# Optimization experiments

Hardware: AMD Instinct MI355X
Metric: run time of the kernel (lower is better)

Reference implementation:

```python
import jax, jax.numpy as jnp
import numpy as np

INNER = 4
AFFECT_W = 0.3
LN_EPS = 1e-5


def _ln(x, w, b):
    m = x.mean(-1, keepdims=True)
    v = ((x - m) ** 2).mean(-1, keepdims=True)
    return (x - m) * jax.lax.rsqrt(v + LN_EPS) * w + b


def _gelu(x):
    return jax.nn.gelu(x, approximate=False)  # torch default erf GELU


def setup_inputs() -> dict:
    key = jax.random.key(0)
    ks = jax.random.split(key, 24)
    B, D = 32768, 128
    s = 0.02
    inp = {
        "x": jax.random.normal(ks[0], (B, D), jnp.float32),
        "y_init": jax.random.normal(ks[1], (B, D), jnp.float32),
        "affect_vec": jax.random.normal(ks[2], (B, 3), jnp.float32),
        # LayerNorms
        "ln_lat_w": jnp.ones((3 * D,), jnp.float32), "ln_lat_b": jnp.zeros((3 * D,), jnp.float32),
        "ln_ans_w": jnp.ones((2 * D,), jnp.float32), "ln_ans_b": jnp.zeros((2 * D,), jnp.float32),
        "ln_z_w": jnp.ones((D,), jnp.float32), "ln_z_b": jnp.zeros((D,), jnp.float32),
        # latent MLP: 3D -> 2D -> D
        "W_lat1": jax.random.normal(ks[3], (3 * D, 2 * D), jnp.float32) * s, "b_lat1": jnp.zeros((2 * D,), jnp.float32),
        "W_lat2": jax.random.normal(ks[4], (2 * D, D), jnp.float32) * s, "b_lat2": jnp.zeros((D,), jnp.float32),
        # answer MLP: 2D -> 2D -> D
        "W_ans1": jax.random.normal(ks[5], (2 * D, 2 * D), jnp.float32) * s, "b_ans1": jnp.zeros((2 * D,), jnp.float32),
        "W_ans2": jax.random.normal(ks[6], (2 * D, D), jnp.float32) * s, "b_ans2": jnp.zeros((D,), jnp.float32),
        # affect proj 3 -> D (tanh), gate 2D -> 1 (sigmoid)
        "W_ap": jax.random.normal(ks[7], (3, D), jnp.float32) * s, "b_ap": jnp.zeros((D,), jnp.float32),
        "W_ag": jax.random.normal(ks[8], (2 * D, 1), jnp.float32) * s, "b_ag": jnp.zeros((1,), jnp.float32),
        # tiny single-head self-attention (q,k,v projections)
        "Wq": jax.random.normal(ks[9], (D, D), jnp.float32) * s, "bq": jnp.zeros((D,), jnp.float32),
        "Wk": jax.random.normal(ks[10], (D, D), jnp.float32) * s, "bk": jnp.zeros((D,), jnp.float32),
        "Wv": jax.random.normal(ks[11], (D, D), jnp.float32) * s, "bv": jnp.zeros((D,), jnp.float32),
        "W_p1": jax.random.normal(ks[12], (D, D // 2), jnp.float32) * s, "b_p1": jnp.zeros((D // 2,), jnp.float32),
        "W_p2": jax.random.normal(ks[13], (D // 2, 3), jnp.float32) * s, "b_p2": jnp.zeros((3,), jnp.float32),
        "K": 5,
    }
    return inp


def reference(x, y_init, affect_vec,
              ln_lat_w, ln_lat_b, ln_ans_w, ln_ans_b, ln_z_w, ln_z_b,
              W_lat1, b_lat1, W_lat2, b_lat2,
              W_ans1, b_ans1, W_ans2, b_ans2,
              W_ap, b_ap, W_ag, b_ag,
              Wq, bq, Wk, bk, Wv, bv,
              W_p1, b_p1, W_p2, b_p2, K):
    D = x.shape[-1]
    scale = 1.0 / jnp.sqrt(jnp.asarray(D, x.dtype))
    y = y_init
    z = jnp.zeros_like(y)
    confs = []
    history = []  # list of [B,1,D]
    for k in range(K):
        for n in range(INNER):
            li = _ln(jnp.concatenate([x, y, z], axis=-1), ln_lat_w, ln_lat_b)
            z_delta = _gelu(li @ W_lat1 + b_lat1) @ W_lat2 + b_lat2
            z = _ln(z + 0.3 * z_delta, ln_z_w, ln_z_b)
        affect_latent = jnp.tanh(affect_vec @ W_ap + b_ap)          # [B,D]
        gate = jax.nn.sigmoid(jnp.concatenate([z, affect_latent], axis=-1) @ W_ag + b_ag)  # [B,1]
        z = z + AFFECT_W * gate * affect_latent
        confs.append(gate.mean())
        history.append(z[:, None, :])
        if len(history) > 1:
            seq = jnp.concatenate(history, axis=1)                   # [B,t,D], t<=K
            q = seq @ Wq + bq
            kk = seq @ Wk + bk
            v = seq @ Wv + bv
            att = jax.nn.softmax(jnp.einsum('btd,bsd->bts', q, kk) * scale, axis=-1)
            attn_out = jnp.einsum('bts,bsd->btd', att, v)
            z = _ln(z + attn_out[:, -1, :], ln_z_w, ln_z_b)
        ai = _ln(jnp.concatenate([y, z], axis=-1), ln_ans_w, ln_ans_b)
        y = y + 0.4 * (_gelu(ai @ W_ans1 + b_ans1) @ W_ans2 + b_ans2)
    pad = jnp.tanh(_gelu(z @ W_p1 + b_p1) @ W_p2 + b_p2)             # [B,3]
    return y, jnp.stack(confs), pad
```

## Files before the change

kernel.cpp:

```cpp
#include <hip/hip_runtime.h>
#include <hip/hip_bf16.h>
#include <math.h>


constexpr int NB = 32768;
constexpr int ND = 128;
constexpr float LNEPS = 1e-5f;

typedef short bf16x8 __attribute__((ext_vector_type(8)));
typedef float f32x4 __attribute__((ext_vector_type(4)));
typedef unsigned uint4v __attribute__((ext_vector_type(4)));
using bf16 = __hip_bfloat16;

static __device__ __forceinline__ float gelu_erf(float x) {
  return 0.5f * x * (1.0f + erff(x * 0.70710678118654752440f));
}
static __device__ __forceinline__ float sigmoidf_(float x) {
  return 1.0f / (1.0f + expf(-x));
}
static __device__ __forceinline__ f32x4 mfma16(bf16x8 a, bf16x8 b, f32x4 c) {
  return __builtin_amdgcn_mfma_f32_16x16x32_bf16(a, b, c, 0, 0, 0);
}
static __device__ __forceinline__ float bfs2f(short u) {
  unsigned v = ((unsigned)(unsigned short)u) << 16;
  return __builtin_bit_cast(float, v);
}
static __device__ __forceinline__ unsigned pk_bf2(float a, float b) {
  unsigned ua = __builtin_bit_cast(unsigned, a);
  unsigned ub = __builtin_bit_cast(unsigned, b);
  ua = (ua + 0x7fffu + ((ua >> 16) & 1u)) >> 16;
  ub = (ub + 0x7fffu + ((ub >> 16) & 1u)) & 0xffff0000u;
  return ub | ua;
}

__global__ void prep_w_frag(const float* __restrict__ src, bf16* __restrict__ dst,
                            int K, int N) {
  int i = blockIdx.x * 256 + threadIdx.x;
  if (i >= K * N) return;
  int k = i / N, n = i - k * N;
  int f = ((n >> 4) * (K >> 5) + (k >> 5)) * 512 + (n & 15) * 32 + (k & 31);
  dst[f] = __float2bfloat16(src[i]);
}

__global__ void prep_w1p(const float* __restrict__ W1, const float* __restrict__ lnw,
                         bf16* __restrict__ WXY, bf16* __restrict__ WZ) {
  int i = blockIdx.x * 256 + threadIdx.x;
  if (i >= 384 * 256) return;
  int j = i >> 8, n = i & 255;
  float v = lnw[j] * W1[i];
  if (j < 256) {
    int f = ((n >> 4) * 8 + (j >> 5)) * 512 + (n & 15) * 32 + (j & 31);
    WXY[f] = __float2bfloat16(v);
  } else {
    int k = j - 256;
    int f = ((n >> 4) * 4 + (k >> 5)) * 512 + (n & 15) * 32 + (k & 31);
    WZ[f] = __float2bfloat16(v);
  }
}

__global__ void prep_uv(const float* __restrict__ W1, const float* __restrict__ lnw,
                        const float* __restrict__ lnb, const float* __restrict__ b1,
                        float* __restrict__ U, float* __restrict__ V0b) {
  int n = threadIdx.x;
  float u = 0.f, v = 0.f;
  for (int j = 0; j < 384; ++j) {
    float w = W1[j * 256 + n];
    u = fmaf(lnw[j], w, u);
    v = fmaf(lnb[j], w, v);
  }
  U[n] = u;
  V0b[n] = v + b1[n];
}

__global__ __launch_bounds__(512) void trm_step(
    const float* __restrict__ x, float* __restrict__ y,
    float* __restrict__ z,
    const bf16* __restrict__ W1XYF, const bf16* __restrict__ W1ZF,
    const float* __restrict__ U, const float* __restrict__ V0b,
    const bf16* __restrict__ W2F, const float* __restrict__ b2,
    const float* __restrict__ lzw, const float* __restrict__ lzb,
    const float* __restrict__ av_g,
    const float* __restrict__ lnw_ans, const float* __restrict__ lnb_ans,
    const bf16* __restrict__ WA1F, const float* __restrict__ ba1,
    const bf16* __restrict__ WA2F, const float* __restrict__ ba2,
    const float* __restrict__ Wap, const float* __restrict__ bap,
    const float* __restrict__ Wag, const float* __restrict__ bag,
    const bf16* __restrict__ WqF, const float* __restrict__ bq,
    const bf16* __restrict__ WkF, const float* __restrict__ bk,
    const bf16* __restrict__ WvF, const float* __restrict__ bv,
    float* __restrict__ gate_sum,
    bf16* __restrict__ kh, bf16* __restrict__ vh, int k)
{
  __shared__ __align__(16) char pool[153600];
  __shared__ float gsum[8];
  float (* const zs)[132] = (float(*)[132])pool;
  float (* const ys)[132] = (float(*)[132])(pool + 33792);
  char* const scr = pool + 67584;
  bf16* const pxy  = (bf16*)scr;
  bf16* const znbL = (bf16*)(scr + 33792);
  bf16* const hx   = (bf16*)(scr + 51200);
  bf16* const znbT = (bf16*)scr;
  bf16* const qvb  = (bf16*)(scr + 17408);
  bf16* const kcb  = (bf16*)(scr + 34816);
  bf16* const vcb  = (bf16*)(scr + 52224);
  bf16* const ai   = (bf16*)scr;
  bf16* const ha   = (bf16*)(scr + 33792);
  float2* const sxy = (float2*)(pool + 152576);
  float2* const mr  = (float2*)(pool + 153088);

  const int t = threadIdx.x;
  const int wave = t >> 6, lane = t & 63;
  const int row8 = t >> 3, sub8 = t & 7;
  const int arow = lane & 15, kseg = (lane >> 4) * 8, crow = (lane >> 4) * 4;
  const size_t row0 = (size_t)blockIdx.x * 64;
  const size_t gr = row0 + row8;

  {
    float s = 0.f, ss = 0.f;
    float4 xv[4], yv[4];
    const float4* xp = (const float4*)&x[gr * ND + sub8 * 16];
    const float4* yp = (const float4*)&y[gr * ND + sub8 * 16];
#pragma unroll
    for (int q = 0; q < 4; ++q) { xv[q] = xp[q]; yv[q] = yp[q]; }
#pragma unroll
    for (int q = 0; q < 4; ++q) {
      s += xv[q].x + xv[q].y + xv[q].z + xv[q].w +
           yv[q].x + yv[q].y + yv[q].z + yv[q].w;
      ss += xv[q].x * xv[q].x + xv[q].y * xv[q].y + xv[q].z * xv[q].z + xv[q].w * xv[q].w +
            yv[q].x * yv[q].x + yv[q].y * yv[q].y + yv[q].z * yv[q].z + yv[q].w * yv[q].w;
    }
#pragma unroll
    for (int q = 0; q < 4; ++q) {
      *(unsigned*)&hx[row8 * 264 + sub8 * 16 + q * 4]       = pk_bf2(xv[q].x, xv[q].y);
      *(unsigned*)&hx[row8 * 264 + sub8 * 16 + q * 4 + 2]   = pk_bf2(xv[q].z, xv[q].w);
      *(unsigned*)&hx[row8 * 264 + 128 + sub8 * 16 + q * 4]     = pk_bf2(yv[q].x, yv[q].y);
      *(unsigned*)&hx[row8 * 264 + 128 + sub8 * 16 + q * 4 + 2] = pk_bf2(yv[q].z, yv[q].w);
      *(float4*)&ys[row8][sub8 * 16 + q * 4] = yv[q];
    }
#pragma unroll
    for (int o = 1; o < 8; o <<= 1) { s += __shfl_xor(s, o); ss += __shfl_xor(ss, o); }

    float zsum = 0.f, zss = 0.f;
    float4 zv[4];
    const float4* zp = (const float4*)&z[gr * ND + sub8 * 16];
#pragma unroll
    for (int q = 0; q < 4; ++q) zv[q] = zp[q];
#pragma unroll
    for (int q = 0; q < 4; ++q) {
      *(float4*)&zs[row8][sub8 * 16 + q * 4] = zv[q];
      *(unsigned*)&znbL[row8 * 136 + sub8 * 16 + q * 4]     = pk_bf2(zv[q].x, zv[q].y);
      *(unsigned*)&znbL[row8 * 136 + sub8 * 16 + q * 4 + 2] = pk_bf2(zv[q].z, zv[q].w);
      zsum += zv[q].x + zv[q].y + zv[q].z + zv[q].w;
      zss += zv[q].x * zv[q].x + zv[q].y * zv[q].y + zv[q].z * zv[q].z + zv[q].w * zv[q].w;
    }
#pragma unroll
    for (int o = 1; o < 8; o <<= 1) { zsum += __shfl_xor(zsum, o); zss += __shfl_xor(zss, o); }
    if (sub8 == 0) {
      sxy[row8] = make_float2(s, ss);
      float mm = (s + zsum) * (1.f / 384.f);
      float var = (ss + zss) * (1.f / 384.f) - mm * mm;
      mr[row8] = make_float2(mm, rsqrtf(var + LNEPS));
    }
  }
  __syncthreads();

  {
    f32x4 acc[4][2];
#pragma unroll
    for (int mi = 0; mi < 4; ++mi)
#pragma unroll
      for (int ni = 0; ni < 2; ++ni) acc[mi][ni] = (f32x4){0.f, 0.f, 0.f, 0.f};
#pragma unroll
    for (int kt = 0; kt < 8; ++kt) {
      bf16x8 a[4];
#pragma unroll
      for (int mi = 0; mi < 4; ++mi)
        a[mi] = *(const bf16x8*)&hx[(mi * 16 + arow) * 264 + kt * 32 + kseg];
#pragma unroll
      for (int ni = 0; ni < 2; ++ni) {
        bf16x8 b = *(const bf16x8*)&W1XYF[(size_t)((wave * 2 + ni) * 8 + kt) * 512 +
                                          arow * 32 + kseg];
        acc[0][ni] = mfma16(a[0], b, acc[0][ni]);
        acc[1][ni] = mfma16(a[1], b, acc[1][ni]);
        acc[2][ni] = mfma16(a[2], b, acc[2][ni]);
        acc[3][ni] = mfma16(a[3], b, acc[3][ni]);
      }
    }
#pragma unroll
    for (int ni = 0; ni < 2; ++ni) {
      int col = (wave * 2 + ni) * 16 + arow;
#pragma unroll
      for (int mi = 0; mi < 4; ++mi)
#pragma unroll
        for (int r = 0; r < 4; ++r)
          pxy[(mi * 16 + crow + r) * 264 + col] = __float2bfloat16(acc[mi][ni][r]);
    }
  }
  __syncthreads();

  float Uv[2], Vv[2];
#pragma unroll
  for (int ni = 0; ni < 2; ++ni) {
    int col = (wave * 2 + ni) * 16 + arow;
    Uv[ni] = U[col];
    Vv[ni] = V0b[col];
  }
  const float b2v = b2[wave * 16 + arow];

  for (int n = 0; n < 4; ++n) {
    {
      f32x4 acc[4][2];
#pragma unroll
      for (int mi = 0; mi < 4; ++mi)
#pragma unroll
        for (int ni = 0; ni < 2; ++ni) acc[mi][ni] = (f32x4){0.f, 0.f, 0.f, 0.f};
#pragma unroll
      for (int kt = 0; kt < 4; ++kt) {
        bf16x8 a[4];
#pragma unroll
        for (int mi = 0; mi < 4; ++mi)
          a[mi] = *(const bf16x8*)&znbL[(mi * 16 + arow) * 136 + kt * 32 + kseg];
#pragma unroll
        for (int ni = 0; ni < 2; ++ni) {
          bf16x8 b = *(const bf16x8*)&W1ZF[(size_t)((wave * 2 + ni) * 4 + kt) * 512 +
                                           arow * 32 + kseg];
          acc[0][ni] = mfma16(a[0], b, acc[0][ni]);
          acc[1][ni] = mfma16(a[1], b, acc[1][ni]);
          acc[2][ni] = mfma16(a[2], b, acc[2][ni]);
          acc[3][ni] = mfma16(a[3], b, acc[3][ni]);
        }
      }
#pragma unroll
      for (int ni = 0; ni < 2; ++ni) {
        int col = (wave * 2 + ni) * 16 + arow;
#pragma unroll
        for (int mi = 0; mi < 4; ++mi)
#pragma unroll
          for (int r = 0; r < 4; ++r) {
            int row = mi * 16 + crow + r;
            float2 mrv = mr[row];
            float pv = __bfloat162float(pxy[row * 264 + col]);
            float hpre = mrv.y * (acc[mi][ni][r] + pv - mrv.x * Uv[ni]) + Vv[ni];
            hx[row * 264 + col] = __float2bfloat16(gelu_erf(hpre));
          }
      }
    }
    __syncthreads();

    {
      f32x4 acc2[4];
#pragma unroll
      for (int mi = 0; mi < 4; ++mi) acc2[mi] = (f32x4){0.f, 0.f, 0.f, 0.f};
#pragma unroll
      for (int kt = 0; kt < 8; ++kt) {
        bf16x8 b = *(const bf16x8*)&W2F[(size_t)(wave * 8 + kt) * 512 + arow * 32 + kseg];
#pragma unroll
        for (int mi = 0; mi < 4; ++mi) {
          bf16x8 a = *(const bf16x8*)&hx[(mi * 16 + arow) * 264 + kt * 32 + kseg];
          acc2[mi] = mfma16(a, b, acc2[mi]);
        }
      }
      int col = wave * 16 + arow;
#pragma unroll
      for (int mi = 0; mi < 4; ++mi)
#pragma unroll
        for (int r = 0; r < 4; ++r)
          zs[mi * 16 + crow + r][col] += 0.3f * (acc2[mi][r] + b2v);
    }
    __syncthreads();

    {
      float4 v[4];
#pragma unroll
      for (int q = 0; q < 4; ++q) v[q] = *(const float4*)&zs[row8][sub8 * 16 + q * 4];
      float s = 0.f, ss = 0.f;
#pragma unroll
      for (int q = 0; q < 4; ++q) {
        s += v[q].x + v[q].y + v[q].z + v[q].w;
        ss += v[q].x * v[q].x + v[q].y * v[q].y + v[q].z * v[q].z + v[q].w * v[q].w;
      }
#pragma unroll
      for (int o = 1; o < 8; o <<= 1) { s += __shfl_xor(s, o); ss += __shfl_xor(ss, o); }
      float m = s * (1.f / 128.f);
      float rstd = rsqrtf(ss * (1.f / 128.f) - m * m + LNEPS);
      float os = 0.f, oss = 0.f;
#pragma unroll
      for (int q = 0; q < 4; ++q) {
        float4 w = *(const float4*)&lzw[sub8 * 16 + q * 4];
        float4 b = *(const float4*)&lzb[sub8 * 16 + q * 4];
        float4 o4;
        o4.x = (v[q].x - m) * rstd * w.x + b.x;
        o4.y = (v[q].y - m) * rstd * w.y + b.y;
        o4.z = (v[q].z - m) * rstd * w.z + b.z;
        o4.w = (v[q].w - m) * rstd * w.w + b.w;
        *(float4*)&zs[row8][sub8 * 16 + q * 4] = o4;
        *(unsigned*)&znbL[row8 * 136 + sub8 * 16 + q * 4]     = pk_bf2(o4.x, o4.y);
        *(unsigned*)&znbL[row8 * 136 + sub8 * 16 + q * 4 + 2] = pk_bf2(o4.z, o4.w);
        os += o4.x + o4.y + o4.z + o4.w;
        oss += o4.x * o4.x + o4.y * o4.y + o4.z * o4.z + o4.w * o4.w;
      }
#pragma unroll
      for (int o = 1; o < 8; o <<= 1) { os += __shfl_xor(os, o); oss += __shfl_xor(oss, o); }
      if (sub8 == 0) {
        float2 sv = sxy[row8];
        float mm = (sv.x + os) * (1.f / 384.f);
        float var = (sv.y + oss) * (1.f / 384.f) - mm * mm;
        mr[row8] = make_float2(mm, rsqrtf(var + LNEPS));
      }
    }
    __syncthreads();
  }

  {
    float zf[16];
#pragma unroll
    for (int q = 0; q < 4; ++q) {
      float4 v = *(const float4*)&zs[row8][sub8 * 16 + q * 4];
      zf[q * 4 + 0] = v.x; zf[q * 4 + 1] = v.y;
      zf[q * 4 + 2] = v.z; zf[q * 4 + 3] = v.w;
    }
    float a0 = av_g[gr * 3 + 0], a1 = av_g[gr * 3 + 1], a2 = av_g[gr * 3 + 2];
    float alf[16];
    float s = 0.f;
#pragma unroll
    for (int e = 0; e < 16; ++e) {
      int c = sub8 * 16 + e;
      alf[e] = tanhf(fmaf(a0, Wap[c], fmaf(a1, Wap[128 + c], fmaf(a2, Wap[256 + c], bap[c]))));
      s += zf[e] * Wag[c] + alf[e] * Wag[128 + c];
    }
#pragma unroll
    for (int o = 1; o < 8; o <<= 1) s += __shfl_xor(s, o);
    float g = sigmoidf_(s + bag[0]);
    float gv = (sub8 == 0) ? g : 0.f;
#pragma unroll
    for (int o = 1; o < 64; o <<= 1) gv += __shfl_xor(gv, o);
    if (lane == 0) gsum[wave] = gv;
#pragma unroll
    for (int e = 0; e < 16; ++e) zf[e] = fmaf(0.3f * g, alf[e], zf[e]);
#pragma unroll
    for (int q = 0; q < 4; ++q) {
      float4 o4;
      o4.x = zf[q * 4 + 0]; o4.y = zf[q * 4 + 1];
      o4.z = zf[q * 4 + 2]; o4.w = zf[q * 4 + 3];
      *(float4*)&zs[row8][sub8 * 16 + q * 4] = o4;
      *(unsigned*)&znbT[row8 * 136 + sub8 * 16 + q * 4]     = pk_bf2(o4.x, o4.y);
      *(unsigned*)&znbT[row8 * 136 + sub8 * 16 + q * 4 + 2] = pk_bf2(o4.z, o4.w);
    }
  }
  __syncthreads();
  if (t == 0) {
    float gs = 0.f;
#pragma unroll
    for (int w = 0; w < 8; ++w) gs += gsum[w];
    atomicAdd(gate_sum + k, gs);
  }

  {
    f32x4 aq[4], ak[4], av2[4];
#pragma unroll
    for (int mi = 0; mi < 4; ++mi) {
      aq[mi] = (f32x4){0.f, 0.f, 0.f, 0.f};
      ak[mi] = (f32x4){0.f, 0.f, 0.f, 0.f};
      av2[mi] = (f32x4){0.f, 0.f, 0.f, 0.f};
    }
#pragma unroll
    for (int kt = 0; kt < 4; ++kt) {
      size_t wr = (size_t)(wave * 4 + kt) * 512 + arow * 32 + kseg;
      bf16x8 bqv = *(const bf16x8*)&WqF[wr];
      bf16x8 bkv = *(const bf16x8*)&WkF[wr];
      bf16x8 bvv = *(const bf16x8*)&WvF[wr];
#pragma unroll
      for (int mi = 0; mi < 4; ++mi) {
        bf16x8 a = *(const bf16x8*)&znbT[(mi * 16 + arow) * 136 + kt * 32 + kseg];
        aq[mi] = mfma16(a, bqv, aq[mi]);
        ak[mi] = mfma16(a, bkv, ak[mi]);
        av2[mi] = mfma16(a, bvv, av2[mi]);
      }
    }
    int col = wave * 16 + arow;
    float bqs = bq[col], bks = bk[col], bvs = bv[col];
#pragma unroll
    for (int mi = 0; mi < 4; ++mi)
#pragma unroll
      for (int r = 0; r < 4; ++r) {
        int row = mi * 16 + crow + r;
        qvb[row * 136 + col] = __float2bfloat16(aq[mi][r] + bqs);
        kcb[row * 136 + col] = __float2bfloat16(ak[mi][r] + bks);
        vcb[row * 136 + col] = __float2bfloat16(av2[mi][r] + bvs);
      }
  }
  __syncthreads();

  if (k < 4) {
    uint4v k0 = *(const uint4v*)&kcb[row8 * 136 + sub8 * 16];
    uint4v k1 = *(const uint4v*)&kcb[row8 * 136 + sub8 * 16 + 8];
    uint4v v0 = *(const uint4v*)&vcb[row8 * 136 + sub8 * 16];
    uint4v v1 = *(const uint4v*)&vcb[row8 * 136 + sub8 * 16 + 8];
    size_t off = ((size_t)k * NB + gr) * ND + sub8 * 16;
    __builtin_nontemporal_store(k0, (uint4v*)&kh[off]);
    __builtin_nontemporal_store(k1, (uint4v*)&kh[off + 8]);
    __builtin_nontemporal_store(v0, (uint4v*)&vh[off]);
    __builtin_nontemporal_store(v1, (uint4v*)&vh[off + 8]);
  }
  {
    float zf[16];
#pragma unroll
    for (int q = 0; q < 4; ++q) {
      float4 v = *(const float4*)&zs[row8][sub8 * 16 + q * 4];
      zf[q * 4 + 0] = v.x; zf[q * 4 + 1] = v.y;
      zf[q * 4 + 2] = v.z; zf[q * 4 + 3] = v.w;
    }
    if (k > 0) {
      bf16x8 qv0 = *(const bf16x8*)&qvb[row8 * 136 + sub8 * 16];
      bf16x8 qv1 = *(const bf16x8*)&qvb[row8 * 136 + sub8 * 16 + 8];
      float p[5];
#pragma unroll
      for (int s = 0; s < 5; ++s) {
        if (s > k) break;
        bf16x8 k0, k1;
        if (s == k) {
          k0 = *(const bf16x8*)&kcb[row8 * 136 + sub8 * 16];
          k1 = *(const bf16x8*)&kcb[row8 * 136 + sub8 * 16 + 8];
        } else {
          size_t off = ((size_t)s * NB + gr) * ND + sub8 * 16;
          k0 = __builtin_bit_cast(bf16x8, __builtin_nontemporal_load((const uint4v*)&kh[off]));
          k1 = __builtin_bit_cast(bf16x8, __builtin_nontemporal_load((const uint4v*)&kh[off + 8]));
        }
        float d = 0.f;
#pragma unroll
        for (int e = 0; e < 8; ++e)
          d += bfs2f(qv0[e]) * bfs2f(k0[e]) + bfs2f(qv1[e]) * bfs2f(k1[e]);
#pragma unroll
        for (int o = 1; o < 8; o <<= 1) d += __shfl_xor(d, o);
        p[s] = d * 0.088388347648318447f;
      }
      float mx = p[0];
#pragma unroll
      for (int s = 1; s < 5; ++s) if (s <= k) mx = fmaxf(mx, p[s]);
      float sum = 0.f;
#pragma unroll
      for (int s = 0; s < 5; ++s) if (s <= k) { p[s] = expf(p[s] - mx); sum += p[s]; }
      float inv = 1.f / sum;
      float ao[16];
#pragma unroll
      for (int e = 0; e < 16; ++e) ao[e] = 0.f;
#pragma unroll
      for (int s = 0; s < 5; ++s) {
        if (s > k) break;
        bf16x8 v0, v1;
        if (s == k) {
          v0 = *(const bf16x8*)&vcb[row8 * 136 + sub8 * 16];
          v1 = *(const bf16x8*)&vcb[row8 * 136 + sub8 * 16 + 8];
        } else {
          size_t off = ((size_t)s * NB + gr) * ND + sub8 * 16;
          v0 = __builtin_bit_cast(bf16x8, __builtin_nontemporal_load((const uint4v*)&vh[off]));
          v1 = __builtin_bit_cast(bf16x8, __builtin_nontemporal_load((const uint4v*)&vh[off + 8]));
        }
        float w = p[s] * inv;
#pragma unroll
        for (int e = 0; e < 8; ++e) {
          ao[e]     = fmaf(w, bfs2f(v0[e]), ao[e]);
          ao[8 + e] = fmaf(w, bfs2f(v1[e]), ao[8 + e]);
        }
      }
#pragma unroll
      for (int e = 0; e < 16; ++e) zf[e] += ao[e];
      float s2 = 0.f, ss = 0.f;
#pragma unroll
      for (int e = 0; e < 16; ++e) { s2 += zf[e]; ss += zf[e] * zf[e]; }
#pragma unroll
      for (int o = 1; o < 8; o <<= 1) { s2 += __shfl_xor(s2, o); ss += __shfl_xor(ss, o); }
      float m = s2 * (1.f / 128.f);
      float rstd = rsqrtf(ss * (1.f / 128.f) - m * m + LNEPS);
#pragma unroll
      for (int e = 0; e < 16; ++e) {
        int c = sub8 * 16 + e;
        zf[e] = (zf[e] - m) * rstd * lzw[c] + lzb[c];
      }
#pragma unroll
      for (int q = 0; q < 4; ++q) {
        float4 o4;
        o4.x = zf[q * 4 + 0]; o4.y = zf[q * 4 + 1];
        o4.z = zf[q * 4 + 2]; o4.w = zf[q * 4 + 3];
        *(float4*)&zs[row8][sub8 * 16 + q * 4] = o4;
      }
    }
#pragma unroll
    for (int q = 0; q < 4; ++q) {
      float4 o4;
      o4.x = zf[q * 4 + 0]; o4.y = zf[q * 4 + 1];
      o4.z = zf[q * 4 + 2]; o4.w = zf[q * 4 + 3];
      *(float4*)&z[gr * ND + sub8 * 16 + q * 4] = o4;
    }
  }
  __syncthreads();

  {
    float yf[16], zf[16];
#pragma unroll
    for (int q = 0; q < 4; ++q) {
      float4 v = *(const float4*)&ys[row8][sub8 * 16 + q * 4];
      yf[q * 4 + 0] = v.x; yf[q * 4 + 1] = v.y;
      yf[q * 4 + 2] = v.z; yf[q * 4 + 3] = v.w;
      float4 w = *(const float4*)&zs[row8][sub8 * 16 + q * 4];
      zf[q * 4 + 0] = w.x; zf[q * 4 + 1] = w.y;
      zf[q * 4 + 2] = w.z; zf[q * 4 + 3] = w.w;
    }
    float s = 0.f, ss = 0.f;
#pragma unroll
    for (int e = 0; e < 16; ++e) {
      s += yf[e] + zf[e];
      ss += yf[e] * yf[e] + zf[e] * zf[e];
    }
#pragma unroll
    for (int o = 1; o < 8; o <<= 1) { s += __shfl_xor(s, o); ss += __shfl_xor(ss, o); }
    float m = s * (1.f / 256.f);
    float rstd = rsqrtf(ss * (1.f / 256.f) - m * m + LNEPS);
#pragma unroll
    for (int h = 0; h < 2; ++h) {
      const float* vp = (h == 0) ? yf : zf;
#pragma unroll
      for (int q = 0; q < 4; ++q) {
        int c0 = h * 128 + sub8 * 16 + q * 4;
        float a0 = (vp[q * 4 + 0] - m) * rstd * lnw_ans[c0 + 0] + lnb_ans[c0 + 0];
        float a1 = (vp[q * 4 + 1] - m) * rstd * lnw_ans[c0 + 1] + lnb_ans[c0 + 1];
        float a2 = (vp[q * 4 + 2] - m) * rstd * lnw_ans[c0 + 2] + lnb_ans[c0 + 2];
        float a3 = (vp[q * 4 + 3] - m) * rstd * lnw_ans[c0 + 3] + lnb_ans[c0 + 3];
        *(unsigned*)&ai[row8 * 264 + c0]     = pk_bf2(a0, a1);
        *(unsigned*)&ai[row8 * 264 + c0 + 2] = pk_bf2(a2, a3);
      }
    }
  }
  __syncthreads();

  {
    f32x4 acc[4][2];
#pragma unroll
    for (int mi = 0; mi < 4; ++mi)
#pragma unroll
      for (int ni = 0; ni < 2; ++ni) acc[mi][ni] = (f32x4){0.f, 0.f, 0.f, 0.f};
#pragma unroll
    for (int kt = 0; kt < 8; ++kt) {
      bf16x8 a[4];
#pragma unroll
      for (int mi = 0; mi < 4; ++mi)
        a[mi] = *(const bf16x8*)&ai[(mi * 16 + arow) * 264 + kt * 32 + kseg];
#pragma unroll
      for (int ni = 0; ni < 2; ++ni) {
        bf16x8 b = *(const bf16x8*)&WA1F[(size_t)((wave * 2 + ni) * 8 + kt) * 512 +
                                         arow * 32 + kseg];
        acc[0][ni] = mfma16(a[0], b, acc[0][ni]);
        acc[1][ni] = mfma16(a[1], b, acc[1][ni]);
        acc[2][ni] = mfma16(a[2], b, acc[2][ni]);
        acc[3][ni] = mfma16(a[3], b, acc[3][ni]);
      }
    }
#pragma unroll
    for (int ni = 0; ni < 2; ++ni) {
      int col = (wave * 2 + ni) * 16 + arow;
      float bb = ba1[col];
#pragma unroll
      for (int mi = 0; mi < 4; ++mi)
#pragma unroll
        for (int r = 0; r < 4; ++r)
          ha[(mi * 16 + crow + r) * 264 + col] =
              __float2bfloat16(gelu_erf(acc[mi][ni][r] + bb));
    }
  }
  __syncthreads();

  {
    f32x4 acc[4];
#pragma unroll
    for (int mi = 0; mi < 4; ++mi) acc[mi] = (f32x4){0.f, 0.f, 0.f, 0.f};
#pragma unroll
    for (int kt = 0; kt < 8; ++kt) {
      bf16x8 b = *(const bf16x8*)&WA2F[(size_t)(wave * 8 + kt) * 512 + arow * 32 + kseg];
#pragma unroll
      for (int mi = 0; mi < 4; ++mi) {
        bf16x8 a = *(const bf16x8*)&ha[(mi * 16 + arow) * 264 + kt * 32 + kseg];
        acc[mi] = mfma16(a, b, acc[mi]);
      }
    }
    int col = wave * 16 + arow;
    float bb = ba2[col];
#pragma unroll
    for (int mi = 0; mi < 4; ++mi)
#pragma unroll
      for (int r = 0; r < 4; ++r)
        ys[mi * 16 + crow + r][col] += 0.4f * (acc[mi][r] + bb);
  }
  __syncthreads();

#pragma unroll
  for (int q = 0; q < 4; ++q)
    *(float4*)&y[gr * ND + sub8 * 16 + q * 4] =
        *(const float4*)&ys[row8][sub8 * 16 + q * 4];
}

__global__ __launch_bounds__(256) void pad_head(
    const float* __restrict__ z,
    const float* __restrict__ W1, const float* __restrict__ b1,
    const float* __restrict__ W2, const float* __restrict__ b2,
    float* __restrict__ out)
{
  __shared__ __align__(16) float zsm[32][132];
  __shared__ __align__(16) float h[32][68];
  const int t = threadIdx.x;
  const int row0 = blockIdx.x * 32;
  {
    const int c = t & 127, rg = t >> 7;
#pragma unroll
    for (int r16 = 0; r16 < 16; ++r16) {
      int r = rg * 16 + r16;
      zsm[r][c] = z[(size_t)(row0 + r) * ND + c];
    }
  }
  __syncthreads();
  {
    const int c = t & 63, rg8 = t >> 6;
    float acc[8];
#pragma unroll
    for (int r = 0; r < 8; ++r) acc[r] = 0.f;
    for (int j0 = 0; j0 < ND; j0 += 4) {
      float w0 = W1[(j0 + 0) * 64 + c], w1 = W1[(j0 + 1) * 64 + c];
      float w2 = W1[(j0 + 2) * 64 + c], w3 = W1[(j0 + 3) * 64 + c];
#pragma unroll
      for (int r = 0; r < 8; ++r) {
        float4 a = *reinterpret_cast<const float4*>(&zsm[rg8 * 8 + r][j0]);
        acc[r] = fmaf(a.x, w0, fmaf(a.y, w1, fmaf(a.z, w2, fmaf(a.w, w3, acc[r]))));
      }
    }
    float bb = b1[c];
#pragma unroll
    for (int r = 0; r < 8; ++r) h[rg8 * 8 + r][c] = gelu_erf(acc[r] + bb);
  }
  __syncthreads();
  {
    const int row = t >> 3, sub = t & 7;
    if (sub < 3) {
      float p = 0.f;
      for (int j = 0; j < 64; ++j) p += h[row][j] * W2[j * 3 + sub];
      out[(size_t)(row0 + row) * 3 + sub] = tanhf(p + b2[sub]);
    }
  }
}

__global__ void finalize_confs(const float* __restrict__ gs, float* __restrict__ confs) {
  int i = threadIdx.x;
  if (i < 5) confs[i] = gs[i] * (1.0f / 32768.0f);
}

extern "C" void kernel_launch(void* const* d_in, const int* in_sizes, int n_in,
                              void* d_out, int out_size, void* d_ws, size_t ws_size,
                              hipStream_t stream) {
  const float* x       = (const float*)d_in[0];
  const float* y_init  = (const float*)d_in[1];
  const float* av      = (const float*)d_in[2];
  const float* ln_lat_w = (const float*)d_in[3];
  const float* ln_lat_b = (const float*)d_in[4];
  const float* ln_ans_w = (const float*)d_in[5];
  const float* ln_ans_b = (const float*)d_in[6];
  const float* ln_z_w   = (const float*)d_in[7];
  const float* ln_z_b   = (const float*)d_in[8];
  const float* W_lat1 = (const float*)d_in[9];  const float* b_lat1 = (const float*)d_in[10];
  const float* W_lat2 = (const float*)d_in[11]; const float* b_lat2 = (const float*)d_in[12];
  const float* W_ans1 = (const float*)d_in[13]; const float* b_ans1 = (const float*)d_in[14];
  const float* W_ans2 = (const float*)d_in[15]; const float* b_ans2 = (const float*)d_in[16];
  const float* W_ap = (const float*)d_in[17];   const float* b_ap = (const float*)d_in[18];
  const float* W_ag = (const float*)d_in[19];   const float* b_ag = (const float*)d_in[20];
  const float* Wq = (const float*)d_in[21];     const float* bq = (const float*)d_in[22];
  const float* Wk = (const float*)d_in[23];     const float* bk = (const float*)d_in[24];
  const float* Wv = (const float*)d_in[25];     const float* bv = (const float*)d_in[26];
  const float* W_p1 = (const float*)d_in[27];   const float* b_p1 = (const float*)d_in[28];
  const float* W_p2 = (const float*)d_in[29];   const float* b_p2 = (const float*)d_in[30];

  float* y     = (float*)d_out;
  float* confs = (float*)d_out + (size_t)NB * ND;
  float* pad   = confs + 5;

  char* p = (char*)d_ws;
  float* gate_sum = (float*)p;
  float* z   = (float*)(p + 256);
  bf16* kh   = (bf16*)(p + 256 + (size_t)NB * ND * 4);
  bf16* vh   = kh + (size_t)4 * NB * ND;
  bf16* W2F  = vh + (size_t)4 * NB * ND;
  bf16* WA1F = W2F + 256 * 128;
  bf16* WA2F = WA1F + 256 * 256;
  bf16* WqF  = WA2F + 256 * 128;
  bf16* WkF  = WqF + 128 * 128;
  bf16* WvF  = WkF + 128 * 128;
  bf16* W1XYF = WvF + 128 * 128;
  bf16* W1ZF  = W1XYF + 256 * 256;
  float* U    = (float*)(W1ZF + 128 * 256);
  float* V0b  = U + 256;

  hipMemcpyAsync(y, y_init, (size_t)NB * ND * sizeof(float),
                 hipMemcpyDeviceToDevice, stream);
  hipMemsetAsync(gate_sum, 0, 32, stream);
  hipMemsetAsync(z, 0, (size_t)NB * ND * sizeof(float), stream);

  prep_w1p<<<(384 * 256 + 255) / 256, 256, 0, stream>>>(W_lat1, ln_lat_w, W1XYF, W1ZF);
  prep_uv<<<1, 256, 0, stream>>>(W_lat1, ln_lat_w, ln_lat_b, b_lat1, U, V0b);
  prep_w_frag<<<(256 * 128 + 255) / 256, 256, 0, stream>>>(W_lat2, W2F, 256, 128);
  prep_w_frag<<<(256 * 256 + 255) / 256, 256, 0, stream>>>(W_ans1, WA1F, 256, 256);
  prep_w_frag<<<(256 * 128 + 255) / 256, 256, 0, stream>>>(W_ans2, WA2F, 256, 128);
  prep_w_frag<<<(128 * 128 + 255) / 256, 256, 0, stream>>>(Wq, WqF, 128, 128);
  prep_w_frag<<<(128 * 128 + 255) / 256, 256, 0, stream>>>(Wk, WkF, 128, 128);
  prep_w_frag<<<(128 * 128 + 255) / 256, 256, 0, stream>>>(Wv, WvF, 128, 128);

  for (int k = 0; k < 5; ++k) {
    trm_step<<<NB / 64, 512, 0, stream>>>(
        x, y, z, W1XYF, W1ZF, U, V0b, W2F, b_lat2, ln_z_w, ln_z_b,
        av, ln_ans_w, ln_ans_b,
        WA1F, b_ans1, WA2F, b_ans2,
        W_ap, b_ap, W_ag, b_ag,
        WqF, bq, WkF, bk, WvF, bv,
        gate_sum, kh, vh, k);
  }
  pad_head<<<NB / 32, 256, 0, stream>>>(z, W_p1, b_p1, W_p2, b_p2, pad);
  finalize_confs<<<1, 64, 0, stream>>>(gate_sum, confs);
}
```

Measured before the change: 800.7 us.

## Keep pxy and weights in registers, prefetch KV history, fuse affect into last inner step

The xy partial product of the latent MLP now stays in MFMA accumulator registers instead of being written to shared memory as bf16. The W1Z and W2 weight fragments are loaded once into registers rather than on every inner iteration. That shared-memory saving shrinks the pool and adds a launch bound of 2 blocks/SM, and the affect/gate stage is folded into the final inner iteration, removing a barrier and a reload of z. The kh/vh history loads are issued early so their latency overlaps the Q/K/V MFMAs. The cost is much higher register pressure, with possible spills under the tighter launch bound, and pxy now stays in fp32 instead of being rounded to bf16.

```diff
diff --git a/kernel.cpp b/kernel.cpp
--- a/kernel.cpp
+++ b/kernel.cpp
@@ -72,7 +72,7 @@
   V0b[n] = v + b1[n];
 }
 
-__global__ __launch_bounds__(512) void trm_step(
+__global__ __launch_bounds__(512, 2) void trm_step(
     const float* __restrict__ x, float* __restrict__ y,
     float* __restrict__ z,
     const bf16* __restrict__ W1XYF, const bf16* __restrict__ W1ZF,
@@ -91,22 +91,21 @@
     float* __restrict__ gate_sum,
     bf16* __restrict__ kh, bf16* __restrict__ vh, int k)
 {
-  __shared__ __align__(16) char pool[153600];
+  __shared__ __align__(16) char pool[138240];
   __shared__ float gsum[8];
   float (* const zs)[132] = (float(*)[132])pool;
   float (* const ys)[132] = (float(*)[132])(pool + 33792);
   char* const scr = pool + 67584;
-  bf16* const pxy  = (bf16*)scr;
-  bf16* const znbL = (bf16*)(scr + 33792);
-  bf16* const hx   = (bf16*)(scr + 51200);
+  bf16* const znbL = (bf16*)scr;
+  bf16* const hx   = (bf16*)(scr + 17408);
   bf16* const znbT = (bf16*)scr;
   bf16* const qvb  = (bf16*)(scr + 17408);
   bf16* const kcb  = (bf16*)(scr + 34816);
   bf16* const vcb  = (bf16*)(scr + 52224);
   bf16* const ai   = (bf16*)scr;
   bf16* const ha   = (bf16*)(scr + 33792);
-  float2* const sxy = (float2*)(pool + 152576);
-  float2* const mr  = (float2*)(pool + 153088);
+  float2* const sxy = (float2*)(pool + 137216);
+  float2* const mr  = (float2*)(pool + 137728);
 
   const int t = threadIdx.x;
   const int wave = t >> 6, lane = t & 63;
@@ -115,6 +114,8 @@
   const size_t row0 = (size_t)blockIdx.x * 64;
   const size_t gr = row0 + row8;
 
+  uint4v khr[4][2], vhr[4][2];
+
   {
     float s = 0.f, ss = 0.f;
     float4 xv[4], yv[4];
@@ -164,12 +165,14 @@
   }
   __syncthreads();
 
-  {
-    f32x4 acc[4][2];
+  f32x4 pxyr[4][2];
+  bf16x8 w1zr[2][4];
+  bf16x8 w2r[8];
+  {
 #pragma unroll
     for (int mi = 0; mi < 4; ++mi)
 #pragma unroll
-      for (int ni = 0; ni < 2; ++ni) acc[mi][ni] = (f32x4){0.f, 0.f, 0.f, 0.f};
+      for (int ni = 0; ni < 2; ++ni) pxyr[mi][ni] = (f32x4){0.f, 0.f, 0.f, 0.f};
 #pragma unroll
     for (int kt = 0; kt < 8; ++kt) {
       bf16x8 a[4];
@@ -180,21 +183,21 @@
       for (int ni = 0; ni < 2; ++ni) {
         bf16x8 b = *(const bf16x8*)&W1XYF[(size_t)((wave * 2 + ni) * 8 + kt) * 512 +
                                           arow * 32 + kseg];
-        acc[0][ni] = mfma16(a[0], b, acc[0][ni]);
-        acc[1][ni] = mfma16(a[1], b, acc[1][ni]);
-        acc[2][ni] = mfma16(a[2], b, acc[2][ni]);
-        acc[3][ni] = mfma16(a[3], b, acc[3][ni]);
-      }
-    }
-#pragma unroll
-    for (int ni = 0; ni < 2; ++ni) {
-      int col = (wave * 2 + ni) * 16 + arow;
-#pragma unroll
-      for (int mi = 0; mi < 4; ++mi)
-#pragma unroll
-        for (int r = 0; r < 4; ++r)
-          pxy[(mi * 16 + crow + r) * 264 + col] = __float2bfloat16(acc[mi][ni][r]);
-    }
+        pxyr[0][ni] = mfma16(a[0], b, pxyr[0][ni]);
+        pxyr[1][ni] = mfma16(a[1], b, pxyr[1][ni]);
+        pxyr[2][ni] = mfma16(a[2], b, pxyr[2][ni]);
+        pxyr[3][ni] = mfma16(a[3], b, pxyr[3][ni]);
+      }
+    }
+#pragma unroll
+    for (int ni = 0; ni < 2; ++ni)
+#pragma unroll
+      for (int kt = 0; kt < 4; ++kt)
+        w1zr[ni][kt] = *(const bf16x8*)&W1ZF[(size_t)((wave * 2 + ni) * 4 + kt) * 512 +
+                                             arow * 32 + kseg];
+#pragma unroll
+    for (int kt = 0; kt < 8; ++kt)
+      w2r[kt] = *(const bf16x8*)&W2F[(size_t)(wave * 8 + kt) * 512 + arow * 32 + kseg];
   }
   __syncthreads();
 
@@ -222,12 +225,10 @@
           a[mi] = *(const bf16x8*)&znbL[(mi * 16 + arow) * 136 + kt * 32 + kseg];
 #pragma unroll
         for (int ni = 0; ni < 2; ++ni) {
-          bf16x8 b = *(const bf16x8*)&W1ZF[(size_t)((wave * 2 + ni) * 4 + kt) * 512 +
-                                           arow * 32 + kseg];
-          acc[0][ni] = mfma16(a[0], b, acc[0][ni]);
-          acc[1][ni] = mfma16(a[1], b, acc[1][ni]);
-          acc[2][ni] = mfma16(a[2], b, acc[2][ni]);
-          acc[3][ni] = mfma16(a[3], b, acc[3][ni]);
+          acc[0][ni] = mfma16(a[0], w1zr[ni][kt], acc[0][ni]);
+          acc[1][ni] = mfma16(a[1], w1zr[ni][kt], acc[1][ni]);
+          acc[2][ni] = mfma16(a[2], w1zr[ni][kt], acc[2][ni]);
+          acc[3][ni] = mfma16(a[3], w1zr[ni][kt], acc[3][ni]);
         }
       }
 #pragma unroll
@@ -239,8 +240,7 @@
           for (int r = 0; r < 4; ++r) {
             int row = mi * 16 + crow + r;
             float2 mrv = mr[row];
-            float pv = __bfloat162float(pxy[row * 264 + col]);
-            float hpre = mrv.y * (acc[mi][ni][r] + pv - mrv.x * Uv[ni]) + Vv[ni];
+            float hpre = mrv.y * (acc[mi][ni][r] + pxyr[mi][ni][r] - mrv.x * Uv[ni]) + Vv[ni];
             hx[row * 264 + col] = __float2bfloat16(gelu_erf(hpre));
           }
       }
@@ -253,11 +253,10 @@
       for (int mi = 0; mi < 4; ++mi) acc2[mi] = (f32x4){0.f, 0.f, 0.f, 0.f};
 #pragma unroll
       for (int kt = 0; kt < 8; ++kt) {
-        bf16x8 b = *(const bf16x8*)&W2F[(size_t)(wave * 8 + kt) * 512 + arow * 32 + kseg];
 #pragma unroll
         for (int mi = 0; mi < 4; ++mi) {
           bf16x8 a = *(const bf16x8*)&hx[(mi * 16 + arow) * 264 + kt * 32 + kseg];
-          acc2[mi] = mfma16(a, b, acc2[mi]);
+          acc2[mi] = mfma16(a, w2r[kt], acc2[mi]);
         }
       }
       int col = wave * 16 + arow;
@@ -270,89 +269,93 @@
     __syncthreads();
 
     {
-      float4 v[4];
-#pragma unroll
-      for (int q = 0; q < 4; ++q) v[q] = *(const float4*)&zs[row8][sub8 * 16 + q * 4];
+      float zf[16];
+#pragma unroll
+      for (int q = 0; q < 4; ++q) {
+        float4 v = *(const float4*)&zs[row8][sub8 * 16 + q * 4];
+        zf[q * 4 + 0] = v.x; zf[q * 4 + 1] = v.y;
+        zf[q * 4 + 2] = v.z; zf[q * 4 + 3] = v.w;
+      }
       float s = 0.f, ss = 0.f;
 #pragma unroll
-      for (int q = 0; q < 4; ++q) {
-        s += v[q].x + v[q].y + v[q].z + v[q].w;
-        ss += v[q].x * v[q].x + v[q].y * v[q].y + v[q].z * v[q].z + v[q].w * v[q].w;
-      }
+      for (int e = 0; e < 16; ++e) { s += zf[e]; ss += zf[e] * zf[e]; }
 #pragma unroll
       for (int o = 1; o < 8; o <<= 1) { s += __shfl_xor(s, o); ss += __shfl_xor(ss, o); }
       float m = s * (1.f / 128.f);
       float rstd = rsqrtf(ss * (1.f / 128.f) - m * m + LNEPS);
-      float os = 0.f, oss = 0.f;
-#pragma unroll
-      for (int q = 0; q < 4; ++q) {
-        float4 w = *(const float4*)&lzw[sub8 * 16 + q * 4];
-        float4 b = *(const float4*)&lzb[sub8 * 16 + q * 4];
-        float4 o4;
-        o4.x = (v[q].x - m) * rstd * w.x + b.x;
-        o4.y = (v[q].y - m) * rstd * w.y + b.y;
-        o4.z = (v[q].z - m) * rstd * w.z + b.z;
-        o4.w = (v[q].w - m) * rstd * w.w + b.w;
-        *(float4*)&zs[row8][sub8 * 16 + q * 4] = o4;
-        *(unsigned*)&znbL[row8 * 136 + sub8 * 16 + q * 4]     = pk_bf2(o4.x, o4.y);
-        *(unsigned*)&znbL[row8 * 136 + sub8 * 16 + q * 4 + 2] = pk_bf2(o4.z, o4.w);
-        os += o4.x + o4.y + o4.z + o4.w;
-        oss += o4.x * o4.x + o4.y * o4.y + o4.z * o4.z + o4.w * o4.w;
-      }
-#pragma unroll
-      for (int o = 1; o < 8; o <<= 1) { os += __shfl_xor(os, o); oss += __shfl_xor(oss, o); }
-      if (sub8 == 0) {
-        float2 sv = sxy[row8];
-        float mm = (sv.x + os) * (1.f / 384.f);
-        float var = (sv.y + oss) * (1.f / 384.f) - mm * mm;
-        mr[row8] = make_float2(mm, rsqrtf(var + LNEPS));
+#pragma unroll
+      for (int e = 0; e < 16; ++e) {
+        int c = sub8 * 16 + e;
+        zf[e] = (zf[e] - m) * rstd * lzw[c] + lzb[c];
+      }
+      if (n < 3) {
+        float os = 0.f, oss = 0.f;
+#pragma unroll
+        for (int e = 0; e < 16; ++e) { os += zf[e]; oss += zf[e] * zf[e]; }
+#pragma unroll
+        for (int o = 1; o < 8; o <<= 1) { os += __shfl_xor(os, o); oss += __shfl_xor(oss, o); }
+#pragma unroll
+        for (int q = 0; q < 4; ++q) {
+          float4 o4;
+          o4.x = zf[q * 4 + 0]; o4.y = zf[q * 4 + 1];
+          o4.z = zf[q * 4 + 2]; o4.w = zf[q * 4 + 3];
+          *(float4*)&zs[row8][sub8 * 16 + q * 4] = o4;
+          *(unsigned*)&znbL[row8 * 136 + sub8 * 16 + q * 4]     = pk_bf2(o4.x, o4.y);
+          *(unsigned*)&znbL[row8 * 136 + sub8 * 16 + q * 4 + 2] = pk_bf2(o4.z, o4.w);
+        }
+        if (sub8 == 0) {
+          float2 sv = sxy[row8];
+          float mm = (sv.x + os) * (1.f / 384.f);
+          float var = (sv.y + oss) * (1.f / 384.f) - mm * mm;
+          mr[row8] = make_float2(mm, rsqrtf(var + LNEPS));
+        }
+      } else {
+        float a0 = av_g[gr * 3 + 0], a1 = av_g[gr * 3 + 1], a2 = av_g[gr * 3 + 2];
+        float alf[16];
+        float gs = 0.f;
+#pragma unroll
+        for (int e = 0; e < 16; ++e) {
+          int c = sub8 * 16 + e;
+          alf[e] = tanhf(fmaf(a0, Wap[c], fmaf(a1, Wap[128 + c], fmaf(a2, Wap[256 + c], bap[c]))));
+          gs += zf[e] * Wag[c] + alf[e] * Wag[128 + c];
+        }
+#pragma unroll
+        for (int o = 1; o < 8; o <<= 1) gs += __shfl_xor(gs, o);
+        float g = sigmoidf_(gs + bag[0]);
+        float gv = (sub8 == 0) ? g : 0.f;
+#pragma unroll
+        for (int o = 1; o < 64; o <<= 1) gv += __shfl_xor(gv, o);
+        if (lane == 0) gsum[wave] = gv;
+#pragma unroll
+        for (int e = 0; e < 16; ++e) zf[e] = fmaf(0.3f * g, alf[e], zf[e]);
+#pragma unroll
+        for (int q = 0; q < 4; ++q) {
+          float4 o4;
+          o4.x = zf[q * 4 + 0]; o4.y = zf[q * 4 + 1];
+          o4.z = zf[q * 4 + 2]; o4.w = zf[q * 4 + 3];
+          *(float4*)&zs[row8][sub8 * 16 + q * 4] = o4;
+          *(unsigned*)&znbT[row8 * 136 + sub8 * 16 + q * 4]     = pk_bf2(o4.x, o4.y);
+          *(unsigned*)&znbT[row8 * 136 + sub8 * 16 + q * 4 + 2] = pk_bf2(o4.z, o4.w);
+        }
+#pragma unroll
+        for (int s5 = 0; s5 < 4; ++s5) {
+          if (s5 < k) {
+            size_t off = ((size_t)s5 * NB + gr) * ND + sub8 * 16;
+            khr[s5][0] = __builtin_nontemporal_load((const uint4v*)&kh[off]);
+            khr[s5][1] = __builtin_nontemporal_load((const uint4v*)&kh[off + 8]);
+            vhr[s5][0] = __builtin_nontemporal_load((const uint4v*)&vh[off]);
+            vhr[s5][1] = __builtin_nontemporal_load((const uint4v*)&vh[off + 8]);
+          }
+        }
       }
     }
     __syncthreads();
   }
-
-  {
-    float zf[16];
-#pragma unroll
-    for (int q = 0; q < 4; ++q) {
-      float4 v = *(const float4*)&zs[row8][sub8 * 16 + q * 4];
-      zf[q * 4 + 0] = v.x; zf[q * 4 + 1] = v.y;
-      zf[q * 4 + 2] = v.z; zf[q * 4 + 3] = v.w;
-    }
-    float a0 = av_g[gr * 3 + 0], a1 = av_g[gr * 3 + 1], a2 = av_g[gr * 3 + 2];
-    float alf[16];
-    float s = 0.f;
-#pragma unroll
-    for (int e = 0; e < 16; ++e) {
-      int c = sub8 * 16 + e;
-      alf[e] = tanhf(fmaf(a0, Wap[c], fmaf(a1, Wap[128 + c], fmaf(a2, Wap[256 + c], bap[c]))));
-      s += zf[e] * Wag[c] + alf[e] * Wag[128 + c];
-    }
-#pragma unroll
-    for (int o = 1; o < 8; o <<= 1) s += __shfl_xor(s, o);
-    float g = sigmoidf_(s + bag[0]);
-    float gv = (sub8 == 0) ? g : 0.f;
-#pragma unroll
-    for (int o = 1; o < 64; o <<= 1) gv += __shfl_xor(gv, o);
-    if (lane == 0) gsum[wave] = gv;
-#pragma unroll
-    for (int e = 0; e < 16; ++e) zf[e] = fmaf(0.3f * g, alf[e], zf[e]);
-#pragma unroll
-    for (int q = 0; q < 4; ++q) {
-      float4 o4;
-      o4.x = zf[q * 4 + 0]; o4.y = zf[q * 4 + 1];
-      o4.z = zf[q * 4 + 2]; o4.w = zf[q * 4 + 3];
-      *(float4*)&zs[row8][sub8 * 16 + q * 4] = o4;
-      *(unsigned*)&znbT[row8 * 136 + sub8 * 16 + q * 4]     = pk_bf2(o4.x, o4.y);
-      *(unsigned*)&znbT[row8 * 136 + sub8 * 16 + q * 4 + 2] = pk_bf2(o4.z, o4.w);
-    }
-  }
-  __syncthreads();
   if (t == 0) {
-    float gs = 0.f;
-#pragma unroll
-    for (int w = 0; w < 8; ++w) gs += gsum[w];
-    atomicAdd(gate_sum + k, gs);
+    float gsv = 0.f;
+#pragma unroll
+    for (int w = 0; w < 8; ++w) gsv += gsum[w];
+    atomicAdd(gate_sum + k, gsv);
   }
 
   {
@@ -422,9 +425,8 @@
           k0 = *(const bf16x8*)&kcb[row8 * 136 + sub8 * 16];
           k1 = *(const bf16x8*)&kcb[row8 * 136 + sub8 * 16 + 8];
         } else {
-          size_t off = ((size_t)s * NB + gr) * ND + sub8 * 16;
-          k0 = __builtin_bit_cast(bf16x8, __builtin_nontemporal_load((const uint4v*)&kh[off]));
-          k1 = __builtin_bit_cast(bf16x8, __builtin_nontemporal_load((const uint4v*)&kh[off + 8]));
+          k0 = __builtin_bit_cast(bf16x8, khr[s][0]);
+          k1 = __builtin_bit_cast(bf16x8, khr[s][1]);
         }
         float d = 0.f;
 #pragma unroll
@@ -452,9 +454,8 @@
           v0 = *(const bf16x8*)&vcb[row8 * 136 + sub8 * 16];
           v1 = *(const bf16x8*)&vcb[row8 * 136 + sub8 * 16 + 8];
         } else {
-          size_t off = ((size_t)s * NB + gr) * ND + sub8 * 16;
-          v0 = __builtin_bit_cast(bf16x8, __builtin_nontemporal_load((const uint4v*)&vh[off]));
-          v1 = __builtin_bit_cast(bf16x8, __builtin_nontemporal_load((const uint4v*)&vh[off + 8]));
+          v0 = __builtin_bit_cast(bf16x8, vhr[s][0]);
+          v1 = __builtin_bit_cast(bf16x8, vhr[s][1]);
         }
         float w = p[s] * inv;
 #pragma unroll
```

New measurement: 1.050 ms. +31.1%, slower.
